# Optimization experiments

Measured on AMD Instinct MI355X. Metric: run time of the kernel, lower is better.

The kernel has to match this reference:

```python
import jax, jax.numpy as jnp
import numpy as np

B, S, D = 2, 2048, 2048
H, DN, DR, DV = 16, 128, 64, 128   # heads, qk_nope, qk_rope, v_head
Q_LORA, KV_LORA = 1536, 512
DQ = DN + DR                        # qk_head_dim = 192
EPS = 1e-6


def setup_inputs() -> dict:
    key = jax.random.key(0)
    ks = jax.random.split(key, 8)
    s = 0.02  # weight init scale
    hidden_states = jax.random.normal(ks[0], (B, S, D), jnp.float32)
    # RoPE tables (non-interleaved HF style: cat(freqs, freqs)) per position
    inv_freq = 1.0 / (10000.0 ** (np.arange(0, DR, 2, dtype=np.float32) / DR))
    freqs = np.arange(S, dtype=np.float32)[:, None] * inv_freq[None, :]  # [S, DR/2]
    emb = np.concatenate([freqs, freqs], axis=-1)                        # [S, DR]
    cos = jnp.broadcast_to(jnp.asarray(np.cos(emb)), (B, S, DR))
    sin = jnp.broadcast_to(jnp.asarray(np.sin(emb)), (B, S, DR))
    return {
        'hidden_states': hidden_states,
        'cos': cos, 'sin': sin,
        'Wqa': jax.random.normal(ks[1], (D, Q_LORA), jnp.float32) * s,
        'qa_ln_w': jnp.ones((Q_LORA,), jnp.float32),
        'Wqb': jax.random.normal(ks[2], (Q_LORA, H * DQ), jnp.float32) * s,
        'Wkva': jax.random.normal(ks[3], (D, KV_LORA + DR), jnp.float32) * s,
        'kva_ln_w': jnp.ones((KV_LORA,), jnp.float32),
        'Wkvb': jax.random.normal(ks[4], (KV_LORA, H * (DN + DV)), jnp.float32) * s,
        'Wo': jax.random.normal(ks[5], (H * DV, D), jnp.float32) * s,
    }


def _rmsnorm(x, w):
    xf = x.astype(jnp.float32)
    var = jnp.mean(xf * xf, axis=-1, keepdims=True)
    return w * (xf * jax.lax.rsqrt(var + EPS)).astype(x.dtype)


def _rotate_half(x):
    h = x.shape[-1] // 2
    return jnp.concatenate([-x[..., h:], x[..., :h]], axis=-1)


def reference(hidden_states, cos, sin, Wqa, qa_ln_w, Wqb, Wkva, kva_ln_w, Wkvb, Wo):
    b, s, _ = hidden_states.shape
    scaling = DQ ** -0.5

    # Q path: down-proj -> RMSNorm -> up-proj -> [b, H, s, DQ]
    q = _rmsnorm(hidden_states @ Wqa, qa_ln_w) @ Wqb
    q = q.reshape(b, s, H, DQ).transpose(0, 2, 1, 3)
    q_pass, q_rot = q[..., :DN], q[..., DN:]

    # KV path: joint down-proj -> split latent / shared rope key
    ckv = hidden_states @ Wkva                       # [b, s, KV_LORA + DR]
    k_lat, k_rot = ckv[..., :KV_LORA], ckv[..., KV_LORA:]
    kv = _rmsnorm(k_lat, kva_ln_w) @ Wkvb            # [b, s, H*(DN+DV)]
    kv = kv.reshape(b, s, H, DN + DV).transpose(0, 2, 1, 3)
    k_pass, v = kv[..., :DN], kv[..., DN:]

    # decoupled RoPE on q_rot and the single shared k_rot head
    k_rot = k_rot[:, None, :, :]                     # [b, 1, s, DR]
    c, si = cos[:, None], sin[:, None]               # unsqueeze_dim=1
    q_rot = q_rot * c + _rotate_half(q_rot) * si
    k_rot = k_rot * c + _rotate_half(k_rot) * si
    k_rot = jnp.broadcast_to(k_rot, (b, H, s, DR))

    Q = jnp.concatenate([q_pass, q_rot], axis=-1)    # [b, H, s, DQ]
    K = jnp.concatenate([k_pass, k_rot], axis=-1)

    scores = jnp.einsum('bhqd,bhkd->bhqk', Q, K) * scaling
    neg = jnp.finfo(jnp.float32).min
    causal = jnp.where(jnp.tril(jnp.ones((s, s), bool)), 0.0, neg)
    scores = scores + causal
    w = jax.nn.softmax(scores.astype(jnp.float32), axis=-1).astype(Q.dtype)

    out = jnp.einsum('bhqk,bhkd->bhqd', w, v)
    out = out.transpose(0, 2, 1, 3).reshape(b, s, H * DV)
    return out @ Wo
```

## Files before the change

### kernel.cpp

```cpp
#include <hip/hip_runtime.h>
#include <math.h>

#define BB 2
#define SS 2048
#define DD 2048
#define HH 16
#define DN 128
#define DR 64
#define DV 128
#define QL 1536
#define KVL 512
#define DQ 192
#define CKVS 640
#define KVD 256
#define NCAT 2176
#define NCATP 2304
#define EPSF 1e-6f

typedef short bfrag __attribute__((ext_vector_type(8)));
typedef float facc  __attribute__((ext_vector_type(4)));

__device__ __forceinline__ ushort f2bf(float f) {
    union { float f; unsigned u; } v; v.f = f;
    unsigned r = v.u + 0x7fffu + ((v.u >> 16) & 1u);
    return (ushort)(r >> 16);
}
__device__ __forceinline__ float bf2f(ushort u) {
    union { unsigned u; float f; } v; v.u = ((unsigned)u) << 16;
    return v.f;
}
__device__ __forceinline__ float fexp2(float x) {
    float r; asm("v_exp_f32 %0, %1" : "=v"(r) : "v"(x)); return r;
}
__device__ __forceinline__ float wave_red_sum(float v) {
    #pragma unroll
    for (int o = 32; o > 0; o >>= 1) v += __shfl_down(v, o);
    return v;
}
__device__ __forceinline__ void gl2lds16(const ushort* g, ushort* l) {
    __builtin_amdgcn_global_load_lds(
        (const __attribute__((address_space(1))) void*)g,
        (__attribute__((address_space(3))) void*)l, 16, 0, 0);
}

__global__ __launch_bounds__(256) void castf2bf(const float* __restrict__ x,
                                                ushort* __restrict__ y) {
    const int i = blockIdx.x * 256 + threadIdx.x;
    const float4 v = ((const float4*)x)[i];
    ushort4 o;
    o.x = f2bf(v.x); o.y = f2bf(v.y); o.z = f2bf(v.z); o.w = f2bf(v.w);
    ((ushort4*)y)[i] = o;
}

struct WtBatch {
    const float* src[5];
    ushort* dst[5];
    int K[5];
    int N[5];
    int nx[5];
    int base[6];
};
__global__ __launch_bounds__(256) void wtrans_b(WtBatch d) {
    __shared__ float tile[32][33];
    int bid = blockIdx.x;
    int seg = 0;
    while (bid >= d.base[seg + 1]) ++seg;
    const int l = bid - d.base[seg];
    const int nx = d.nx[seg];
    const int bx = l % nx, by = l / nx;
    const float* W = d.src[seg];
    ushort* Wt = d.dst[seg];
    const int K = d.K[seg], N = d.N[seg];
    const int k0 = by * 32, n0 = bx * 32;
    const int t = threadIdx.x;
    const int tx = t & 31, ty = t >> 5;
    #pragma unroll
    for (int r = 0; r < 4; ++r) {
        const int n = n0 + tx;
        tile[ty + r * 8][tx] =
            (n < N) ? W[(size_t)(k0 + ty + r * 8) * N + n] : 0.f;
    }
    __syncthreads();
    #pragma unroll
    for (int r = 0; r < 4; ++r) {
        const int n = n0 + ty + r * 8;
        Wt[(size_t)n * K + k0 + tx] = f2bf(tile[tx][ty + r * 8]);
    }
}


__device__ __forceinline__ void stage_half(const ushort* __restrict__ G,
                                           int ldg, int grow0, int kcol0,
                                           ushort* Lr, int wave, int lane) {
    const int r0   = lane >> 3;
    const int slot = (lane & 7) ^ r0;
    const ushort* s0 = G + (size_t)(grow0 + wave * 16 + r0) * ldg + kcol0 + slot * 8;
    gl2lds16(s0,                    Lr + wave * 1024);
    gl2lds16(s0 + (size_t)8 * ldg,  Lr + wave * 1024 + 512);
}

#define PH_PRE  do { __builtin_amdgcn_sched_barrier(0);                      \
                     __builtin_amdgcn_s_barrier();                           \
                     asm volatile("s_waitcnt lgkmcnt(0)" ::: "memory");      \
                     __builtin_amdgcn_sched_barrier(0);                      \
                     __builtin_amdgcn_s_setprio(1); } while (0)
#define PH_POST do { __builtin_amdgcn_s_setprio(0);                          \
                     __builtin_amdgcn_sched_barrier(0);                      \
                     __builtin_amdgcn_s_barrier(); } while (0)

#define MFMA16(RB)                                                           \
    _Pragma("unroll")                                                        \
    for (int i = 0; i < 4; ++i)                                              \
        _Pragma("unroll")                                                    \
        for (int j = 0; j < 4; ++j)                                          \
            acc[(RB) + i][j] = __builtin_amdgcn_mfma_f32_16x16x32_bf16(      \
                a[i], b[j], acc[(RB) + i][j], 0, 0, 0);

#define GEMM256_CORE(A_, Bt_, K_, NBX_, LID_)                                 \
    const int t    = threadIdx.x;                                             \
    const int lane = t & 63;                                                  \
    const int wave = t >> 6;                                                  \
    const int wm   = wave >> 2;                                               \
    const int wn   = wave & 3;                                                \
    const int quad = lane >> 4;                                               \
    const int lrow = lane & 15;                                               \
    const int bx = (LID_) % (NBX_), by = (LID_) / (NBX_);                     \
    const int m0 = by * 256, n0 = bx * 256;                                   \
    const int s0x8  = (quad ^ (lrow & 7)) * 8;       \
    const int s1x8  = s0x8 ^ 32;                   \
    const int abase = lrow * 64;                                              \
    const int bbase = (wn & 1) * 4096 + lrow * 64;                            \
    facc acc[8][4];                                                           \
    _Pragma("unroll")                                                         \
    for (int i = 0; i < 8; ++i)                                               \
        _Pragma("unroll")                                                     \
        for (int j = 0; j < 4; ++j) acc[i][j] = (facc)(0.f);                  \
    const int nk = (K_) >> 6;                                                 \
                  \
    stage_half((A_),  (K_), m0,        0, L,         wave, lane);             \
    stage_half((A_),  (K_), m0 + 128,  0, L + 8192,  wave, lane);             \
    stage_half((Bt_), (K_), n0,        0, L + 16384, wave, lane);             \
    stage_half((Bt_), (K_), n0 + 128,  0, L + 24576, wave, lane);             \
    stage_half((Bt_), (K_), n0,       64, L + 49152, wave, lane);             \
    stage_half((Bt_), (K_), n0 + 128, 64, L + 57344, wave, lane);             \
    asm volatile("s_waitcnt vmcnt(4)" ::: "memory");                          \
    __builtin_amdgcn_s_barrier();                                             \
    for (int kt = 0; kt < nk; ++kt) {                                         \
        const int p = kt & 1;                                                 \
        ushort* LA = L + p * 32768 + wm * 8192;                               \
        ushort* LB = L + p * 32768 + 16384 + (wn >> 1) * 8192;                \
        ushort* Lq = L + (p ^ 1) * 32768;                                     \
        const int kn = (kt + 1) * 64;                                         \
        bfrag a[4], b[4];                                                     \
                                           \
        _Pragma("unroll")                                                     \
        for (int i = 0; i < 4; ++i)                                           \
            a[i] = *(const bfrag*)(LA + i * 1024 + abase + s0x8);             \
        _Pragma("unroll")                                                     \
        for (int j = 0; j < 4; ++j)                                           \
            b[j] = *(const bfrag*)(LB + bbase + j * 1024 + s0x8);             \
        if (kt + 1 < nk) stage_half((A_), (K_), m0, kn, Lq, wave, lane);      \
        PH_PRE;                                                               \
        MFMA16(0)                                                             \
        PH_POST;                                                              \
                                \
        _Pragma("unroll")                                                     \
        for (int i = 0; i < 4; ++i)                                           \
            a[i] = *(const bfrag*)(LA + (4 + i) * 1024 + abase + s0x8);       \
        if (kt + 1 < nk)                                                      \
            stage_half((A_), (K_), m0 + 128, kn, Lq + 8192, wave, lane);      \
        PH_PRE;                                                               \
        MFMA16(4)                                                             \
        PH_POST;                                                              \
                                           \
        _Pragma("unroll")                                                     \
        for (int i = 0; i < 4; ++i)                                           \
            a[i] = *(const bfrag*)(LA + i * 1024 + abase + s1x8);             \
        _Pragma("unroll")                                                     \
        for (int j = 0; j < 4; ++j)                                           \
            b[j] = *(const bfrag*)(LB + bbase + j * 1024 + s1x8);             \
        PH_PRE;                                                               \
        MFMA16(0)                                                             \
        PH_POST;                                                              \
             \
        _Pragma("unroll")                                                     \
        for (int i = 0; i < 4; ++i)                                           \
            a[i] = *(const bfrag*)(LA + (4 + i) * 1024 + abase + s1x8);       \
        if (kt + 2 < nk) {                                                    \
            stage_half((Bt_), (K_), n0,       kn + 64,                        \
                       L + p * 32768 + 16384, wave, lane);                    \
            stage_half((Bt_), (K_), n0 + 128, kn + 64,                        \
                       L + p * 32768 + 24576, wave, lane);                    \
            asm volatile("s_waitcnt vmcnt(4)" ::: "memory");                  \
        } else {                                                              \
            asm volatile("s_waitcnt vmcnt(0)" ::: "memory");                  \
        }                                                                     \
        PH_PRE;                                                               \
        MFMA16(4)                                                             \
        PH_POST;                                                              \
    }

template <int K, int NBX, int NOUT>
__global__ __launch_bounds__(512, 2) void gemmW(const ushort* __restrict__ A,
                                                const ushort* __restrict__ Bt,
                                                float* __restrict__ C) {
    __shared__ ushort L[57344];
    const int t    = threadIdx.x;
    const int lane = t & 63;
    const int wave = t >> 6;
    const int wm   = wave >> 1;
    const int wn   = wave & 1;
    const int quad = lane >> 4;
    const int lrow = lane & 15;
    int wg = (int)blockIdx.x;
    { const int cpx = (int)gridDim.x >> 3; wg = (wg & 7) * cpx + (wg >> 3); }
    const int bx = wg % NBX, by = wg / NBX;
    const int m0 = by * 256, n0 = bx * 128;
    const int s0x8 = (quad ^ (lrow & 7)) * 8;
    const int s1x8 = s0x8 ^ 32;
    facc acc[4][4];
    #pragma unroll
    for (int i = 0; i < 4; ++i)
        #pragma unroll
        for (int j = 0; j < 4; ++j) acc[i][j] = (facc)(0.f);
    const int nk = K >> 6;
    stage_half(A,  K, m0,        0, L,          wave, lane);
    stage_half(A,  K, m0 + 128,  0, L + 8192,   wave, lane);
    stage_half(Bt, K, n0,        0, L + 32768,  wave, lane);
    stage_half(Bt, K, n0,       64, L + 40960,  wave, lane);
    asm volatile("s_waitcnt vmcnt(0)" ::: "memory");
    __builtin_amdgcn_s_barrier();
    int bp = 0, bp2 = 2;
    for (int kt = 0; kt < nk; ++kt) {
        const int p = kt & 1;
        ushort* LA = L + p * 16384 + (wm >> 1) * 8192
                       + ((wm & 1) * 64 + lrow) * 64;
        ushort* LB = L + 32768 + bp * 8192 + (wn * 64 + lrow) * 64;
        const int kn = (kt + 1) * 64;
        bfrag a[4], b[4];
        #pragma unroll
        for (int i = 0; i < 4; ++i) a[i] = *(const bfrag*)(LA + i * 1024 + s0x8);
        #pragma unroll
        for (int j = 0; j < 4; ++j) b[j] = *(const bfrag*)(LB + j * 1024 + s0x8);
        if (kt + 1 < nk) {
            stage_half(A, K, m0,       kn, L + (p ^ 1) * 16384,        wave, lane);
            stage_half(A, K, m0 + 128, kn, L + (p ^ 1) * 16384 + 8192, wave, lane);
        }
        if (kt + 2 < nk)
            stage_half(Bt, K, n0, kn + 64, L + 32768 + bp2 * 8192, wave, lane);
        PH_PRE;
        MFMA16(0)
        PH_POST;
        #pragma unroll
        for (int i = 0; i < 4; ++i) a[i] = *(const bfrag*)(LA + i * 1024 + s1x8);
        #pragma unroll
        for (int j = 0; j < 4; ++j) b[j] = *(const bfrag*)(LB + j * 1024 + s1x8);
        if (kt + 2 < nk) { asm volatile("s_waitcnt vmcnt(2)" ::: "memory"); }
        else             { asm volatile("s_waitcnt vmcnt(0)" ::: "memory"); }
        PH_PRE;
        MFMA16(0)
        PH_POST;
        bp  = (bp  == 2) ? 0 : bp  + 1;
        bp2 = (bp2 == 2) ? 0 : bp2 + 1;
    }
    #pragma unroll
    for (int m = 0; m < 4; ++m) {
        const int row = m0 + wm * 64 + m * 16 + quad * 4;
        #pragma unroll
        for (int nf = 0; nf < 4; ++nf) {
            const int col = n0 + wn * 64 + nf * 16 + lrow;
            #pragma unroll
            for (int r = 0; r < 4; ++r)
                C[(size_t)(row + r) * NOUT + col] = acc[m][nf][r];
        }
    }
}

__global__ __launch_bounds__(512, 2) void gemmA256(const ushort* __restrict__ A,
                                                   const ushort* __restrict__ Bt,
                                                   ushort* __restrict__ qa,
                                                   ushort* __restrict__ ckv) {
    __shared__ ushort L[65536];
    const int lid = ((int)blockIdx.x & 7) * 18 + ((int)blockIdx.x >> 3);
    GEMM256_CORE(A, Bt, DD, 9, lid)
    #pragma unroll
    for (int m = 0; m < 8; ++m) {
        const int row = m0 + wm * 128 + m * 16 + quad * 4;
        #pragma unroll
        for (int nf = 0; nf < 4; ++nf) {
            const int col = n0 + wn * 64 + nf * 16 + lrow;
            #pragma unroll
            for (int r = 0; r < 4; ++r) {
                if (col < QL)
                    qa[(size_t)(row + r) * QL + col] = f2bf(acc[m][nf][r]);
                else if (col < NCAT)
                    ckv[(size_t)(row + r) * CKVS + col - QL] = f2bf(acc[m][nf][r]);
            }
        }
    }
}

__global__ __launch_bounds__(512, 2) void gemmQKV(
    const ushort* __restrict__ qa,  const ushort* __restrict__ Wqbt,
    ushort* __restrict__ Qbuf,
    const ushort* __restrict__ kvn, const ushort* __restrict__ Wkvbt,
    ushort* __restrict__ kvb) {
    __shared__ ushort L[65536];
    const int bid = (int)blockIdx.x;
    if (bid < 192) {
        const int lid = (bid & 7) * 24 + (bid >> 3);
        GEMM256_CORE(qa, Wqbt, QL, 12, lid)
        const float scaling = 0.10411754831f;
        #pragma unroll
        for (int m = 0; m < 8; ++m) {
            const int row = m0 + wm * 128 + m * 16 + quad * 4;
            #pragma unroll
            for (int nf = 0; nf < 4; ++nf) {
                const int col = n0 + wn * 64 + nf * 16 + lrow;
                const int h = col / DQ, d = col - h * DQ;
                #pragma unroll
                for (int r = 0; r < 4; ++r) {
                    const int tok = row + r;
                    const int b = tok >> 11, s = tok & (SS - 1);
                    Qbuf[((size_t)(b * HH + h) * SS + s) * DQ + d] =
                        f2bf(acc[m][nf][r] * scaling);
                }
            }
        }
    } else {
        const int b2 = bid - 192;
        const int lid = (b2 & 7) * 32 + (b2 >> 3);
        GEMM256_CORE(kvn, Wkvbt, KVL, 16, lid)
        #pragma unroll
        for (int m = 0; m < 8; ++m) {
            const int row = m0 + wm * 128 + m * 16 + quad * 4;
            #pragma unroll
            for (int nf = 0; nf < 4; ++nf) {
                const int col = n0 + wn * 64 + nf * 16 + lrow;
                #pragma unroll
                for (int r = 0; r < 4; ++r)
                    kvb[(size_t)(row + r) * (HH * KVD) + col] = f2bf(acc[m][nf][r]);
            }
        }
    }
}

__global__ __launch_bounds__(256) void rmsnorm2(ushort* __restrict__ qa,
                                                const float* __restrict__ qaw,
                                                const ushort* __restrict__ ckv,
                                                const float* __restrict__ kvw,
                                                ushort* __restrict__ kvn,
                                                ushort* __restrict__ krb,
                                                const float* __restrict__ cosb,
                                                const float* __restrict__ sinb) {
    __shared__ float red[4];
    const int t = threadIdx.x;
    const int lane = t & 63, wid = t >> 6;
    const int bid = (int)blockIdx.x;
    if (bid < BB * SS) {
        ushort* xr = qa + (size_t)bid * QL;
        float ss = 0.f;
        for (int i = t; i < QL; i += 256) { float v = bf2f(xr[i]); ss += v * v; }
        ss = wave_red_sum(ss);
        if (lane == 0) red[wid] = ss;
        __syncthreads();
        const float tot = red[0] + red[1] + red[2] + red[3];
        const float sc = rsqrtf(tot / (float)QL + EPSF);
        for (int i = t; i < QL; i += 256) xr[i] = f2bf(qaw[i] * bf2f(xr[i]) * sc);
    } else {
        const int row = bid - BB * SS;
        const ushort* xr = ckv + (size_t)row * CKVS;
        ushort* yr = kvn + (size_t)row * KVL;
        if (t < 64) {
            const int p = t;
            const ushort* kin = xr + KVL;
            const float c  = cosb[(size_t)row * DR + p];
            const float sn = sinb[(size_t)row * DR + p];
            const float self = bf2f(kin[p]);
            const float partner = bf2f(kin[p < 32 ? p + 32 : p - 32]);
            const float v = (p < 32) ? (self * c - partner * sn)
                                     : (self * c + partner * sn);
            krb[(size_t)row * DR + p] = f2bf(v);
        }
        float ss = 0.f;
        for (int i = t; i < KVL; i += 256) { float v = bf2f(xr[i]); ss += v * v; }
        ss = wave_red_sum(ss);
        if (lane == 0) red[wid] = ss;
        __syncthreads();
        const float tot = red[0] + red[1] + red[2] + red[3];
        const float sc = rsqrtf(tot / (float)KVL + EPSF);
        for (int i = t; i < KVL; i += 256) yr[i] = f2bf(kvw[i] * bf2f(xr[i]) * sc);
    }
}

__global__ __launch_bounds__(256) void ropevprep(ushort* __restrict__ Qbuf,
                                                 const float* __restrict__ cosb,
                                                 const float* __restrict__ sinb,
                                                 const ushort* __restrict__ kvb,
                                                 ushort* __restrict__ Vtb) {
    __shared__ ushort tile[32][33];
    const int bid = (int)blockIdx.x;
    const int t = threadIdx.x;
    if (bid < BB * SS) {
        const int tok = bid;
        const int b = tok >> 11, s = tok & (SS - 1);
        const int p = t & 31, hh = t >> 5;
        const float c0 = cosb[(size_t)tok * DR + p];
        const float s0 = sinb[(size_t)tok * DR + p];
        const float c1 = cosb[(size_t)tok * DR + p + 32];
        const float s1 = sinb[(size_t)tok * DR + p + 32];
        #pragma unroll
        for (int it = 0; it < 2; ++it) {
            const int h = hh + it * 8;
            ushort* base = Qbuf + ((size_t)(b * HH + h) * SS + s) * DQ + DN;
            const float x0 = bf2f(base[p]), x1 = bf2f(base[p + 32]);
            base[p]      = f2bf(x0 * c0 - x1 * s0);
            base[p + 32] = f2bf(x1 * c1 + x0 * s1);
        }
    } else {
        const int v = bid - BB * SS;
        const int kp0 = (v & 63) * 32;
        const int dv0 = ((v >> 6) & 3) * 32;
        const int bh  = v >> 8;
        const int b = bh / HH, h = bh - b * HH;
        const int tx = t & 31, ty = t >> 5;
        #pragma unroll
        for (int r = 0; r < 4; ++r)
            tile[ty + r * 8][tx] =
                kvb[(size_t)(b * SS + kp0 + ty + r * 8) * (HH * KVD) + h * KVD + DN + dv0 + tx];
        __syncthreads();
        #pragma unroll
        for (int r = 0; r < 4; ++r)
            Vtb[((size_t)bh * DV + dv0 + ty + r * 8) * SS + kp0 + tx] = tile[tx][ty + r * 8];
    }
}

__global__ __launch_bounds__(256, 2) void fattn_mfma(
    const ushort* __restrict__ Qb,
    const ushort* __restrict__ kvb,
    const ushort* __restrict__ krb,
    const ushort* __restrict__ Vt,
    ushort* __restrict__ o)
{
    const int h  = blockIdx.y;
    const int b  = blockIdx.z;
    const int qt = b ? (15 - (int)blockIdx.x) : (int)blockIdx.x;
    const int bh = b * HH + h;
    const int q0 = qt * 128;
    const int t    = threadIdx.x;
    const int lane = t & 63;
    const int wave = t >> 6;
    const int quad = lane >> 4;
    const int n    = lane & 15;
    const int wstrip = wave * 16;

    __shared__ ushort Ksu[6 * 64 * 32];
    __shared__ ushort Vtu[2 * 128 * 32];
    __shared__ ushort Psu[2 * 128 * 40];

    const ushort* vbase = Vt + (size_t)bh * DV * SS;

    bfrag aQ[2][6];
    #pragma unroll
    for (int sp = 0; sp < 2; ++sp) {
        const ushort* qrow = Qb + ((size_t)bh * SS + q0 + sp * 64 + wstrip + n) * DQ;
        #pragma unroll
        for (int kb = 0; kb < 6; ++kb)
            aQ[sp][kb] = *(const bfrag*)(qrow + kb * 32 + quad * 8);
    }

    facc oacc[2][8];
    float lp[2][4];
    #pragma unroll
    for (int sp = 0; sp < 2; ++sp) {
        #pragma unroll
        for (int jd = 0; jd < 8; ++jd) oacc[sp][jd] = (facc)(0.f);
        #pragma unroll
        for (int r = 0; r < 4; ++r) lp[sp][r] = 0.f;
    }

    #pragma unroll
    for (int i = 0; i < 6; ++i) {
        const int g = wave + 4 * i;
        const int kb = g >> 2;
        const int rem = (g & 3) * 64 + lane;
        const int row = rem >> 2, sub = rem & 3;
        const int tok = b * SS + row;
        const ushort* src = (kb < 4)
            ? kvb + (size_t)tok * (HH * KVD) + h * KVD + kb * 32 + sub * 8
            : krb + (size_t)tok * DR + (kb - 4) * 32 + sub * 8;
        gl2lds16(src, Ksu + g * 512);
    }
    #pragma unroll
    for (int i = 0; i < 4; ++i) {
        const int g = wave + 4 * i;
        const int kb2 = g >> 3;
        const int rem = (g & 7) * 64 + lane;
        const int dv = rem >> 2, sub = rem & 3;
        gl2lds16(vbase + (size_t)dv * SS + kb2 * 32 + sub * 8, Vtu + g * 512);
    }
    __syncthreads();

    const int nkt = 2 * qt + 2;
    for (int kt = 0; kt < nkt; ++kt) {
        const int k0 = kt * 64;
        const bool more = (kt + 1 < nkt);
        const int kk = more ? (k0 + 64) : (SS - 64);

        bfrag kreg[6], vreg[4];
        #pragma unroll
        for (int i = 0; i < 6; ++i) {
            const int g = wave + 4 * i;
            const int kb = g >> 2;
            const int rem = (g & 3) * 64 + lane;
            const int row = rem >> 2, sub = rem & 3;
            const int tok = b * SS + kk + row;
            const ushort* src = (kb < 4)
                ? kvb + (size_t)tok * (HH * KVD) + h * KVD + kb * 32 + sub * 8
                : krb + (size_t)tok * DR + (kb - 4) * 32 + sub * 8;
            kreg[i] = *(const bfrag*)src;
        }
        #pragma unroll
        for (int i = 0; i < 4; ++i) {
            const int g = wave + 4 * i;
            const int kb2 = g >> 3;
            const int rem = (g & 7) * 64 + lane;
            const int dv = rem >> 2, sub = rem & 3;
            vreg[i] = *(const bfrag*)(vbase + (size_t)dv * SS + kk + kb2 * 32 + sub * 8);
        }
        __builtin_amdgcn_sched_barrier(0);

        facc s[2][4];
        #pragma unroll
        for (int sp = 0; sp < 2; ++sp)
            #pragma unroll
            for (int j = 0; j < 4; ++j) s[sp][j] = (facc)(0.f);
        #pragma unroll
        for (int kb = 0; kb < 6; ++kb) {
            #pragma unroll
            for (int j = 0; j < 4; ++j) {
                const bfrag bk =
                    *(const bfrag*)&Ksu[kb * 2048 + (j * 16 + n) * 32 + quad * 8];
                s[0][j] = __builtin_amdgcn_mfma_f32_16x16x32_bf16(aQ[0][kb], bk, s[0][j], 0, 0, 0);
                s[1][j] = __builtin_amdgcn_mfma_f32_16x16x32_bf16(aQ[1][kb], bk, s[1][j], 0, 0, 0);
            }
        }

        const bool fullt = (k0 + 64 <= q0);
        if (fullt) {
            #pragma unroll
            for (int sp = 0; sp < 2; ++sp) {
                #pragma unroll
                for (int j = 0; j < 4; ++j) {
                    #pragma unroll
                    for (int r = 0; r < 4; ++r) {
                        const float p = fexp2(s[sp][j][r]);
                        lp[sp][r] += p;
                        Psu[(j >> 1) * 5120 + (sp * 64 + wstrip + quad * 4 + r) * 40
                            + (j & 1) * 16 + n] = f2bf(p);
                    }
                }
            }
        } else {
            #pragma unroll
            for (int sp = 0; sp < 2; ++sp) {
                const int rowg0 = q0 + sp * 64 + wstrip + quad * 4;
                #pragma unroll
                for (int j = 0; j < 4; ++j) {
                    const int kpos = k0 + j * 16 + n;
                    #pragma unroll
                    for (int r = 0; r < 4; ++r) {
                        const float p = (kpos <= rowg0 + r) ? fexp2(s[sp][j][r]) : 0.f;
                        lp[sp][r] += p;
                        Psu[(j >> 1) * 5120 + (sp * 64 + wstrip + quad * 4 + r) * 40
                            + (j & 1) * 16 + n] = f2bf(p);
                    }
                }
            }
        }

        #pragma unroll
        for (int kb2 = 0; kb2 < 2; ++kb2) {
            const bfrag aP0 = *(const bfrag*)&Psu[kb2 * 5120 + (wstrip + n) * 40 + quad * 8];
            const bfrag aP1 = *(const bfrag*)&Psu[kb2 * 5120 + (64 + wstrip + n) * 40 + quad * 8];
            #pragma unroll
            for (int jd = 0; jd < 8; ++jd) {
                const bfrag bV = *(const bfrag*)&Vtu[kb2 * 4096 + (jd * 16 + n) * 32 + quad * 8];
                oacc[0][jd] = __builtin_amdgcn_mfma_f32_16x16x32_bf16(aP0, bV, oacc[0][jd], 0, 0, 0);
                oacc[1][jd] = __builtin_amdgcn_mfma_f32_16x16x32_bf16(aP1, bV, oacc[1][jd], 0, 0, 0);
            }
        }

        __syncthreads();
        #pragma unroll
        for (int i = 0; i < 6; ++i)
            *(bfrag*)(Ksu + (wave + 4 * i) * 512 + lane * 8) = kreg[i];
        #pragma unroll
        for (int i = 0; i < 4; ++i)
            *(bfrag*)(Vtu + (wave + 4 * i) * 512 + lane * 8) = vreg[i];
        __syncthreads();
    }

    #pragma unroll
    for (int sp = 0; sp < 2; ++sp) {
        #pragma unroll
        for (int r = 0; r < 4; ++r) {
            float v = lp[sp][r];
            #pragma unroll
            for (int msk = 1; msk < 16; msk <<= 1) v += __shfl_xor(v, msk);
            const float inv = 1.f / v;
            ushort* op = o + (size_t)(b * SS + q0 + sp * 64 + wstrip + quad * 4 + r)
                             * (HH * DV) + h * DV;
            #pragma unroll
            for (int jd = 0; jd < 8; ++jd)
                op[jd * 16 + n] = f2bf(oacc[sp][jd][r] * inv);
        }
    }
}

extern "C" void kernel_launch(void* const* d_in, const int* in_sizes, int n_in,
                              void* d_out, int out_size, void* d_ws, size_t ws_size,
                              hipStream_t stream) {
    const float* hs    = (const float*)d_in[0];
    const float* cosb  = (const float*)d_in[1];
    const float* sinb  = (const float*)d_in[2];
    const float* Wqa   = (const float*)d_in[3];
    const float* qa_w  = (const float*)d_in[4];
    const float* Wqb   = (const float*)d_in[5];
    const float* Wkva  = (const float*)d_in[6];
    const float* kva_w = (const float*)d_in[7];
    const float* Wkvb  = (const float*)d_in[8];
    const float* Wo    = (const float*)d_in[9];
    float* out = (float*)d_out;

    const int T = BB * SS;

    char* w = (char*)d_ws;
    auto alloc = [&](size_t bytes) {
        void* r = (void*)w;
        w += (bytes + 255) & ~(size_t)255;
        return r;
    };
    ushort* hs_bf  = (ushort*)alloc((size_t)T * DD * 2);
    ushort* Wcat   = (ushort*)alloc((size_t)NCATP * DD * 2);
    ushort* Wqbt   = (ushort*)alloc((size_t)(HH * DQ) * QL * 2);
    ushort* Wkvbt  = (ushort*)alloc((size_t)(HH * KVD) * KVL * 2);
    ushort* Wot    = (ushort*)alloc((size_t)DD * DD * 2);
    ushort* qa_bf  = (ushort*)alloc((size_t)T * QL * 2);
    ushort* Qbuf   = (ushort*)alloc((size_t)T * HH * DQ * 2);
    ushort* ckv_bf = (ushort*)alloc((size_t)T * CKVS * 2);
    ushort* kvn_bf = (ushort*)alloc((size_t)T * KVL * 2);
    ushort* kv_bf  = (ushort*)alloc((size_t)T * HH * KVD * 2);
    ushort* krb    = (ushort*)alloc((size_t)T * DR * 2);
    ushort* Vtb    = Wcat;
    ushort* ao_bf  = hs_bf;

    castf2bf<<<(T * DD / 4) / 256, 256, 0, stream>>>(hs, hs_bf);
    WtBatch wb;
    wb.src[0] = Wqa;  wb.dst[0] = Wcat;                      wb.K[0] = DD;  wb.N[0] = QL;       wb.nx[0] = 48;
    wb.src[1] = Wkva; wb.dst[1] = Wcat + (size_t)QL * DD;    wb.K[1] = DD;  wb.N[1] = KVL + DR; wb.nx[1] = 20;
    wb.src[2] = Wqb;  wb.dst[2] = Wqbt;                      wb.K[2] = QL;  wb.N[2] = HH * DQ;  wb.nx[2] = 96;
    wb.src[3] = Wkvb; wb.dst[3] = Wkvbt;                     wb.K[3] = KVL; wb.N[3] = HH * KVD; wb.nx[3] = 128;
    wb.src[4] = Wo;   wb.dst[4] = Wot;                       wb.K[4] = DD;  wb.N[4] = DD;       wb.nx[4] = 64;
    wb.base[0] = 0;
    wb.base[1] = wb.base[0] + wb.nx[0] * (DD / 32);
    wb.base[2] = wb.base[1] + wb.nx[1] * (DD / 32);
    wb.base[3] = wb.base[2] + wb.nx[2] * (QL / 32);
    wb.base[4] = wb.base[3] + wb.nx[3] * (KVL / 32);
    wb.base[5] = wb.base[4] + wb.nx[4] * (DD / 32);
    wtrans_b<<<wb.base[5], 256, 0, stream>>>(wb);

    gemmA256<<<dim3(144), 512, 0, stream>>>(hs_bf, Wcat, qa_bf, ckv_bf);
    rmsnorm2<<<2 * T, 256, 0, stream>>>(qa_bf, qa_w, ckv_bf, kva_w, kvn_bf,
                                        krb, cosb, sinb);
    gemmQKV<<<dim3(448), 512, 0, stream>>>(qa_bf, Wqbt, Qbuf,
                                           kvn_bf, Wkvbt, kv_bf);
    ropevprep<<<T + 8192, 256, 0, stream>>>(Qbuf, cosb, sinb, kv_bf, Vtb);
    fattn_mfma<<<dim3(16, HH, BB), 256, 0, stream>>>(Qbuf, kv_bf, krb, Vtb, ao_bf);
    gemmW<DD, 16, DD><<<dim3(256), 512, 0, stream>>>(ao_bf, Wot, out);
}
```

Baseline: 423.3 us.

## Overlap later weight transposes with first GEMM and retile QKV GEMM to 256x128

The Wqb, Wkvb and Wo transpose/cast work moves out of the standalone transpose kernel and into 112 extra blocks of the first projection GEMM launch, so it runs concurrently with the hidden-state down-projection. Each extra block loops over 32x32 tiles using two half-block tiles in shared memory. Separately, the Q/KV up-projection GEMM switches from 256x256 tiles to the 256x128 tile core used by the output GEMM, doubling the block count to 896 and using less LDS. The aim is to hide the transpose cost behind the GEMM and improve occupancy and load balance in the QKV GEMM, at the cost of transpose blocks competing with the GEMM for bandwidth and CUs.

New measurement: 414.3 us. -2.1%, faster.

```diff
diff --git a/kernel.cpp b/kernel.cpp
--- a/kernel.cpp
+++ b/kernel.cpp
@@ -53,18 +53,17 @@
 }
 
 struct WtBatch {
-    const float* src[5];
-    ushort* dst[5];
-    int K[5];
-    int N[5];
-    int nx[5];
-    int base[6];
+    const float* src[2];
+    ushort* dst[2];
+    int K[2];
+    int N[2];
+    int nx[2];
+    int base[3];
 };
 __global__ __launch_bounds__(256) void wtrans_b(WtBatch d) {
     __shared__ float tile[32][33];
     int bid = blockIdx.x;
-    int seg = 0;
-    while (bid >= d.base[seg + 1]) ++seg;
+    int seg = (bid >= d.base[1]) ? 1 : 0;
     const int l = bid - d.base[seg];
     const int nx = d.nx[seg];
     const int bx = l % nx, by = l / nx;
@@ -136,7 +135,6 @@
         _Pragma("unroll")                                                     \
         for (int j = 0; j < 4; ++j) acc[i][j] = (facc)(0.f);                  \
     const int nk = (K_) >> 6;                                                 \
-                  \
     stage_half((A_),  (K_), m0,        0, L,         wave, lane);             \
     stage_half((A_),  (K_), m0 + 128,  0, L + 8192,  wave, lane);             \
     stage_half((Bt_), (K_), n0,        0, L + 16384, wave, lane);             \
@@ -152,7 +150,6 @@
         ushort* Lq = L + (p ^ 1) * 32768;                                     \
         const int kn = (kt + 1) * 64;                                         \
         bfrag a[4], b[4];                                                     \
-                                           \
         _Pragma("unroll")                                                     \
         for (int i = 0; i < 4; ++i)                                           \
             a[i] = *(const bfrag*)(LA + i * 1024 + abase + s0x8);             \
@@ -163,7 +160,6 @@
         PH_PRE;                                                               \
         MFMA16(0)                                                             \
         PH_POST;                                                              \
-                                \
         _Pragma("unroll")                                                     \
         for (int i = 0; i < 4; ++i)                                           \
             a[i] = *(const bfrag*)(LA + (4 + i) * 1024 + abase + s0x8);       \
@@ -172,7 +168,6 @@
         PH_PRE;                                                               \
         MFMA16(4)                                                             \
         PH_POST;                                                              \
-                                           \
         _Pragma("unroll")                                                     \
         for (int i = 0; i < 4; ++i)                                           \
             a[i] = *(const bfrag*)(LA + i * 1024 + abase + s1x8);             \
@@ -182,7 +177,6 @@
         PH_PRE;                                                               \
         MFMA16(0)                                                             \
         PH_POST;                                                              \
-             \
         _Pragma("unroll")                                                     \
         for (int i = 0; i < 4; ++i)                                           \
             a[i] = *(const bfrag*)(LA + (4 + i) * 1024 + abase + s1x8);       \
@@ -200,69 +194,72 @@
         PH_POST;                                                              \
     }
 
+#define GEMMW_CORE(A_, Bt_, K_, NBX_, LID_)                                   \
+    const int t    = threadIdx.x;                                             \
+    const int lane = t & 63;                                                  \
+    const int wave = t >> 6;                                                  \
+    const int wm   = wave >> 1;                                     \
+    const int wn   = wave & 1;                                      \
+    const int quad = lane >> 4;                                               \
+    const int lrow = lane & 15;                                               \
+    const int bx = (LID_) % (NBX_), by = (LID_) / (NBX_);                     \
+    const int m0 = by * 256, n0 = bx * 128;                                   \
+    const int s0x8 = (quad ^ (lrow & 7)) * 8;                                 \
+    const int s1x8 = s0x8 ^ 32;                                               \
+    facc acc[4][4];                                                           \
+    _Pragma("unroll")                                                         \
+    for (int i = 0; i < 4; ++i)                                               \
+        _Pragma("unroll")                                                     \
+        for (int j = 0; j < 4; ++j) acc[i][j] = (facc)(0.f);                  \
+    const int nk = (K_) >> 6;                                                 \
+    stage_half((A_),  (K_), m0,        0, L,          wave, lane);            \
+    stage_half((A_),  (K_), m0 + 128,  0, L + 8192,   wave, lane);            \
+    stage_half((Bt_), (K_), n0,        0, L + 32768,  wave, lane);            \
+    stage_half((Bt_), (K_), n0,       64, L + 40960,  wave, lane);            \
+    asm volatile("s_waitcnt vmcnt(0)" ::: "memory");                          \
+    __builtin_amdgcn_s_barrier();                                             \
+    int bp = 0, bp2 = 2;                               \
+    for (int kt = 0; kt < nk; ++kt) {                                         \
+        const int p = kt & 1;                                                 \
+        ushort* LA = L + p * 16384 + (wm >> 1) * 8192                         \
+                       + ((wm & 1) * 64 + lrow) * 64;                         \
+        ushort* LB = L + 32768 + bp * 8192 + (wn * 64 + lrow) * 64;           \
+        const int kn = (kt + 1) * 64;                                         \
+        bfrag a[4], b[4];                                                     \
+        _Pragma("unroll")                                                     \
+        for (int i = 0; i < 4; ++i) a[i] = *(const bfrag*)(LA + i * 1024 + s0x8); \
+        _Pragma("unroll")                                                     \
+        for (int j = 0; j < 4; ++j) b[j] = *(const bfrag*)(LB + j * 1024 + s0x8); \
+        if (kt + 1 < nk) {                                                    \
+            stage_half((A_), (K_), m0,       kn, L + (p ^ 1) * 16384,        wave, lane); \
+            stage_half((A_), (K_), m0 + 128, kn, L + (p ^ 1) * 16384 + 8192, wave, lane); \
+        }                                                                     \
+        if (kt + 2 < nk)                                                      \
+            stage_half((Bt_), (K_), n0, kn + 64, L + 32768 + bp2 * 8192, wave, lane); \
+        PH_PRE;                                                               \
+        MFMA16(0)                                                             \
+        PH_POST;                                                              \
+        _Pragma("unroll")                                                     \
+        for (int i = 0; i < 4; ++i) a[i] = *(const bfrag*)(LA + i * 1024 + s1x8); \
+        _Pragma("unroll")                                                     \
+        for (int j = 0; j < 4; ++j) b[j] = *(const bfrag*)(LB + j * 1024 + s1x8); \
+        if (kt + 2 < nk) { asm volatile("s_waitcnt vmcnt(2)" ::: "memory"); } \
+        else             { asm volatile("s_waitcnt vmcnt(0)" ::: "memory"); } \
+        PH_PRE;                                                               \
+        MFMA16(0)                                                             \
+        PH_POST;                                                              \
+        bp  = (bp  == 2) ? 0 : bp  + 1;                                       \
+        bp2 = (bp2 == 2) ? 0 : bp2 + 1;                                       \
+    }
+
 template <int K, int NBX, int NOUT>
 __global__ __launch_bounds__(512, 2) void gemmW(const ushort* __restrict__ A,
                                                 const ushort* __restrict__ Bt,
                                                 float* __restrict__ C) {
     __shared__ ushort L[57344];
-    const int t    = threadIdx.x;
-    const int lane = t & 63;
-    const int wave = t >> 6;
-    const int wm   = wave >> 1;
-    const int wn   = wave & 1;
-    const int quad = lane >> 4;
-    const int lrow = lane & 15;
     int wg = (int)blockIdx.x;
     { const int cpx = (int)gridDim.x >> 3; wg = (wg & 7) * cpx + (wg >> 3); }
-    const int bx = wg % NBX, by = wg / NBX;
-    const int m0 = by * 256, n0 = bx * 128;
-    const int s0x8 = (quad ^ (lrow & 7)) * 8;
-    const int s1x8 = s0x8 ^ 32;
-    facc acc[4][4];
-    #pragma unroll
-    for (int i = 0; i < 4; ++i)
-        #pragma unroll
-        for (int j = 0; j < 4; ++j) acc[i][j] = (facc)(0.f);
-    const int nk = K >> 6;
-    stage_half(A,  K, m0,        0, L,          wave, lane);
-    stage_half(A,  K, m0 + 128,  0, L + 8192,   wave, lane);
-    stage_half(Bt, K, n0,        0, L + 32768,  wave, lane);
-    stage_half(Bt, K, n0,       64, L + 40960,  wave, lane);
-    asm volatile("s_waitcnt vmcnt(0)" ::: "memory");
-    __builtin_amdgcn_s_barrier();
-    int bp = 0, bp2 = 2;
-    for (int kt = 0; kt < nk; ++kt) {
-        const int p = kt & 1;
-        ushort* LA = L + p * 16384 + (wm >> 1) * 8192
-                       + ((wm & 1) * 64 + lrow) * 64;
-        ushort* LB = L + 32768 + bp * 8192 + (wn * 64 + lrow) * 64;
-        const int kn = (kt + 1) * 64;
-        bfrag a[4], b[4];
-        #pragma unroll
-        for (int i = 0; i < 4; ++i) a[i] = *(const bfrag*)(LA + i * 1024 + s0x8);
-        #pragma unroll
-        for (int j = 0; j < 4; ++j) b[j] = *(const bfrag*)(LB + j * 1024 + s0x8);
-        if (kt + 1 < nk) {
-            stage_half(A, K, m0,       kn, L + (p ^ 1) * 16384,        wave, lane);
-            stage_half(A, K, m0 + 128, kn, L + (p ^ 1) * 16384 + 8192, wave, lane);
-        }
-        if (kt + 2 < nk)
-            stage_half(Bt, K, n0, kn + 64, L + 32768 + bp2 * 8192, wave, lane);
-        PH_PRE;
-        MFMA16(0)
-        PH_POST;
-        #pragma unroll
-        for (int i = 0; i < 4; ++i) a[i] = *(const bfrag*)(LA + i * 1024 + s1x8);
-        #pragma unroll
-        for (int j = 0; j < 4; ++j) b[j] = *(const bfrag*)(LB + j * 1024 + s1x8);
-        if (kt + 2 < nk) { asm volatile("s_waitcnt vmcnt(2)" ::: "memory"); }
-        else             { asm volatile("s_waitcnt vmcnt(0)" ::: "memory"); }
-        PH_PRE;
-        MFMA16(0)
-        PH_POST;
-        bp  = (bp  == 2) ? 0 : bp  + 1;
-        bp2 = (bp2 == 2) ? 0 : bp2 + 1;
-    }
+    GEMMW_CORE(A, Bt, K, NBX, wg)
     #pragma unroll
     for (int m = 0; m < 4; ++m) {
         const int row = m0 + wm * 64 + m * 16 + quad * 4;
@@ -276,26 +273,55 @@
     }
 }
 
-__global__ __launch_bounds__(512, 2) void gemmA256(const ushort* __restrict__ A,
-                                                   const ushort* __restrict__ Bt,
-                                                   ushort* __restrict__ qa,
-                                                   ushort* __restrict__ ckv) {
+__global__ __launch_bounds__(512, 2) void gemmAW(
+    const ushort* __restrict__ A,   const ushort* __restrict__ Bt,
+    ushort* __restrict__ qa,        ushort* __restrict__ ckv,
+    const float* __restrict__ Wqb,  ushort* __restrict__ Wqbt,
+    const float* __restrict__ Wkvb, ushort* __restrict__ Wkvbt,
+    const float* __restrict__ Wo,   ushort* __restrict__ Wot) {
     __shared__ ushort L[65536];
-    const int lid = ((int)blockIdx.x & 7) * 18 + ((int)blockIdx.x >> 3);
-    GEMM256_CORE(A, Bt, DD, 9, lid)
-    #pragma unroll
-    for (int m = 0; m < 8; ++m) {
-        const int row = m0 + wm * 128 + m * 16 + quad * 4;
-        #pragma unroll
-        for (int nf = 0; nf < 4; ++nf) {
-            const int col = n0 + wn * 64 + nf * 16 + lrow;
-            #pragma unroll
-            for (int r = 0; r < 4; ++r) {
-                if (col < QL)
-                    qa[(size_t)(row + r) * QL + col] = f2bf(acc[m][nf][r]);
-                else if (col < NCAT)
-                    ckv[(size_t)(row + r) * CKVS + col - QL] = f2bf(acc[m][nf][r]);
+    const int bid = (int)blockIdx.x;
+    if (bid < 144) {
+        const int lid = (bid & 7) * 18 + (bid >> 3);
+        GEMM256_CORE(A, Bt, DD, 9, lid)
+        #pragma unroll
+        for (int m = 0; m < 8; ++m) {
+            const int row = m0 + wm * 128 + m * 16 + quad * 4;
+            #pragma unroll
+            for (int nf = 0; nf < 4; ++nf) {
+                const int col = n0 + wn * 64 + nf * 16 + lrow;
+                #pragma unroll
+                for (int r = 0; r < 4; ++r) {
+                    if (col < QL)
+                        qa[(size_t)(row + r) * QL + col] = f2bf(acc[m][nf][r]);
+                    else if (col < NCAT)
+                        ckv[(size_t)(row + r) * CKVS + col - QL] = f2bf(acc[m][nf][r]);
+                }
             }
+        }
+    } else {
+        const int wid = bid - 144;
+        const int t   = threadIdx.x;
+        const int half = t >> 8;
+        const int tl = t & 255;
+        const int tx = tl & 31, ty = tl >> 5;
+        float (*tile)[33] = (float(*)[33])((float*)L + half * 32 * 33);
+        for (int it = 0; it < 48; ++it) {
+            const int idx = (it * 112 + wid) * 2 + half;
+            const float* W; ushort* Wt; int K, N, nx, l;
+            if (idx < 4608)      { l = idx;        W = Wqb;  Wt = Wqbt;  K = QL;  N = HH * DQ;  nx = 96; }
+            else if (idx < 6656) { l = idx - 4608; W = Wkvb; Wt = Wkvbt; K = KVL; N = HH * KVD; nx = 128; }
+            else                 { l = idx - 6656; W = Wo;   Wt = Wot;   K = DD;  N = DD;       nx = 64; }
+            const int bx2 = l % nx, by2 = l / nx;
+            const int k0 = by2 * 32, n0w = bx2 * 32;
+            #pragma unroll
+            for (int r = 0; r < 4; ++r)
+                tile[ty + r * 8][tx] = W[(size_t)(k0 + ty + r * 8) * N + n0w + tx];
+            __syncthreads();
+            #pragma unroll
+            for (int r = 0; r < 4; ++r)
+                Wt[(size_t)(n0w + ty + r * 8) * K + k0 + tx] = f2bf(tile[tx][ty + r * 8]);
+            __syncthreads();
         }
     }
 }
@@ -305,15 +331,15 @@
     ushort* __restrict__ Qbuf,
     const ushort* __restrict__ kvn, const ushort* __restrict__ Wkvbt,
     ushort* __restrict__ kvb) {
-    __shared__ ushort L[65536];
+    __shared__ ushort L[57344];
     const int bid = (int)blockIdx.x;
-    if (bid < 192) {
-        const int lid = (bid & 7) * 24 + (bid >> 3);
-        GEMM256_CORE(qa, Wqbt, QL, 12, lid)
+    if (bid < 384) {
+        const int lid = (bid & 7) * 48 + (bid >> 3);
+        GEMMW_CORE(qa, Wqbt, QL, 24, lid)
         const float scaling = 0.10411754831f;
         #pragma unroll
-        for (int m = 0; m < 8; ++m) {
-            const int row = m0 + wm * 128 + m * 16 + quad * 4;
+        for (int m = 0; m < 4; ++m) {
+            const int row = m0 + wm * 64 + m * 16 + quad * 4;
             #pragma unroll
             for (int nf = 0; nf < 4; ++nf) {
                 const int col = n0 + wn * 64 + nf * 16 + lrow;
@@ -321,19 +347,19 @@
                 #pragma unroll
                 for (int r = 0; r < 4; ++r) {
                     const int tok = row + r;
-                    const int b = tok >> 11, s = tok & (SS - 1);
-                    Qbuf[((size_t)(b * HH + h) * SS + s) * DQ + d] =
+                    const int b = tok >> 11, s2 = tok & (SS - 1);
+                    Qbuf[((size_t)(b * HH + h) * SS + s2) * DQ + d] =
                         f2bf(acc[m][nf][r] * scaling);
                 }
             }
         }
     } else {
-        const int b2 = bid - 192;
-        const int lid = (b2 & 7) * 32 + (b2 >> 3);
-        GEMM256_CORE(kvn, Wkvbt, KVL, 16, lid)
-        #pragma unroll
-        for (int m = 0; m < 8; ++m) {
-            const int row = m0 + wm * 128 + m * 16 + quad * 4;
+        const int b2 = bid - 384;
+        const int lid = (b2 & 7) * 64 + (b2 >> 3);
+        GEMMW_CORE(kvn, Wkvbt, KVL, 32, lid)
+        #pragma unroll
+        for (int m = 0; m < 4; ++m) {
+            const int row = m0 + wm * 64 + m * 16 + quad * 4;
             #pragma unroll
             for (int nf = 0; nf < 4; ++nf) {
                 const int col = n0 + wn * 64 + nf * 16 + lrow;
@@ -504,8 +530,7 @@
     const int nkt = 2 * qt + 2;
     for (int kt = 0; kt < nkt; ++kt) {
         const int k0 = kt * 64;
-        const bool more = (kt + 1 < nkt);
-        const int kk = more ? (k0 + 64) : (SS - 64);
+        const int kk = (kt + 1 < nkt) ? (k0 + 64) : (SS - 64);
 
         bfrag kreg[6], vreg[4];
         #pragma unroll
@@ -657,23 +682,18 @@
 
     castf2bf<<<(T * DD / 4) / 256, 256, 0, stream>>>(hs, hs_bf);
     WtBatch wb;
-    wb.src[0] = Wqa;  wb.dst[0] = Wcat;                      wb.K[0] = DD;  wb.N[0] = QL;       wb.nx[0] = 48;
-    wb.src[1] = Wkva; wb.dst[1] = Wcat + (size_t)QL * DD;    wb.K[1] = DD;  wb.N[1] = KVL + DR; wb.nx[1] = 20;
-    wb.src[2] = Wqb;  wb.dst[2] = Wqbt;                      wb.K[2] = QL;  wb.N[2] = HH * DQ;  wb.nx[2] = 96;
-    wb.src[3] = Wkvb; wb.dst[3] = Wkvbt;                     wb.K[3] = KVL; wb.N[3] = HH * KVD; wb.nx[3] = 128;
-    wb.src[4] = Wo;   wb.dst[4] = Wot;                       wb.K[4] = DD;  wb.N[4] = DD;       wb.nx[4] = 64;
+    wb.src[0] = Wqa;  wb.dst[0] = Wcat;                   wb.K[0] = DD; wb.N[0] = QL;       wb.nx[0] = 48;
+    wb.src[1] = Wkva; wb.dst[1] = Wcat + (size_t)QL * DD; wb.K[1] = DD; wb.N[1] = KVL + DR; wb.nx[1] = 20;
     wb.base[0] = 0;
-    wb.base[1] = wb.base[0] + wb.nx[0] * (DD / 32);
+    wb.base[1] = wb.nx[0] * (DD / 32);
     wb.base[2] = wb.base[1] + wb.nx[1] * (DD / 32);
-    wb.base[3] = wb.base[2] + wb.nx[2] * (QL / 32);
-    wb.base[4] = wb.base[3] + wb.nx[3] * (KVL / 32);
-    wb.base[5] = wb.base[4] + wb.nx[4] * (DD / 32);
-    wtrans_b<<<wb.base[5], 256, 0, stream>>>(wb);
-
-    gemmA256<<<dim3(144), 512, 0, stream>>>(hs_bf, Wcat, qa_bf, ckv_bf);
+    wtrans_b<<<wb.base[2], 256, 0, stream>>>(wb);
+
+    gemmAW<<<dim3(256), 512, 0, stream>>>(hs_bf, Wcat, qa_bf, ckv_bf,
+                                          Wqb, Wqbt, Wkvb, Wkvbt, Wo, Wot);
     rmsnorm2<<<2 * T, 256, 0, stream>>>(qa_bf, qa_w, ckv_bf, kva_w, kvn_bf,
                                         krb, cosb, sinb);
-    gemmQKV<<<dim3(448), 512, 0, stream>>>(qa_bf, Wqbt, Qbuf,
+    gemmQKV<<<dim3(896), 512, 0, stream>>>(qa_bf, Wqbt, Qbuf,
                                            kvn_bf, Wkvbt, kv_bf);
     ropevprep<<<T + 8192, 256, 0, stream>>>(Qbuf, cosb, sinb, kv_bf, Vtb);
     fattn_mfma<<<dim3(16, HH, BB), 256, 0, stream>>>(Qbuf, kv_bf, krb, Vtb, ao_bf);
```
